# Kernel optimization log

Hardware: AMD Instinct MI355X
Metric: run time of the kernel (lower is better)

Reference implementation:

```python
import jax, jax.numpy as jnp
import numpy as np

N_NODES = 50000
N_EDGES = 800000
D_NODE = 128
D_EDGE = 128
D_OUT = 256
HID = 256


def setup_inputs() -> dict:
    key = jax.random.key(0)
    ks = jax.random.split(key, 10)
    s1 = 1.0 / np.sqrt(D_NODE + D_EDGE)
    s2 = 1.0 / np.sqrt(HID)
    s3 = 1.0 / np.sqrt(D_NODE + HID)
    return {
        "x": jax.random.normal(ks[0], (N_NODES, D_NODE), dtype=jnp.float32),
        "edge_index": jax.random.randint(ks[1], (2, N_EDGES), 0, N_NODES, dtype=jnp.int64),
        "edge_attr": jax.random.normal(ks[2], (N_EDGES, D_EDGE), dtype=jnp.float32),
        "u": jax.random.normal(ks[3], (1, 64), dtype=jnp.float32),
        "batch": jnp.zeros((N_NODES,), dtype=jnp.int64),
        "w1a": jax.random.normal(ks[4], (D_NODE + D_EDGE, HID), dtype=jnp.float32) * s1,
        "b1a": jnp.zeros((HID,), dtype=jnp.float32),
        "w1b": jax.random.normal(ks[5], (HID, HID), dtype=jnp.float32) * s2,
        "b1b": jnp.zeros((HID,), dtype=jnp.float32),
        "w2a": jax.random.normal(ks[6], (D_NODE + HID, HID), dtype=jnp.float32) * s3,
        "b2a": jnp.zeros((HID,), dtype=jnp.float32),
        "w2b": jax.random.normal(ks[7], (HID, D_OUT), dtype=jnp.float32) * s2,
        "b2b": jnp.zeros((D_OUT,), dtype=jnp.float32),
    }


def reference(x, edge_index, edge_attr, u, batch, w1a, b1a, w1b, b1b, w2a, b2a, w2b, b2b):
    row, col = edge_index[0], edge_index[1]
    # edge-wise MLP: [E, D_NODE + D_EDGE] -> 256 -> 256
    h = jnp.concatenate([x[row], edge_attr], axis=1)
    h = jax.nn.elu(h @ w1a + b1a) @ w1b + b1b  # [E, 256]
    # scatter_mean over destination nodes (dim_size = N)
    n = x.shape[0]
    sums = jax.ops.segment_sum(h, col, num_segments=n)  # [N, 256]
    cnt = jax.ops.segment_sum(jnp.ones((h.shape[0],), h.dtype), col, num_segments=n)
    mean = sums / jnp.maximum(cnt, 1.0)[:, None]
    # node-wise MLP: [N, D_NODE + 256] -> 256 -> D_OUT
    z = jnp.concatenate([x, mean], axis=1)
    return jax.nn.elu(z @ w2a + b2a) @ w2b + b2b
```

## Files before the change

kernel.cpp:

```cpp
#include <hip/hip_runtime.h>
#include <hip/hip_bf16.h>

#define N_NODES 50000
#define N_EDGES 800000

typedef short s16x8 __attribute__((ext_vector_type(8)));
typedef short s16x4 __attribute__((ext_vector_type(4)));
typedef float f32x4 __attribute__((ext_vector_type(4)));
typedef unsigned int u32x2 __attribute__((ext_vector_type(2)));

__device__ __forceinline__ unsigned short f2bf(float f) {
    union { float f; unsigned u; } v; v.f = f;
    unsigned r = v.u + 0x7fffu + ((v.u >> 16) & 1u);
    return (unsigned short)(r >> 16);
}

__device__ __forceinline__ unsigned cvt_pk_bf16(float a, float b) {
    unsigned r;
    asm("v_cvt_pk_bf16_f32 %0, %1, %2" : "=v"(r) : "v"(a), "v"(b));
    return r;
}

__device__ __forceinline__ s16x8 ld8(const unsigned short* p) {
    return *(const s16x8*)p;
}

__device__ __forceinline__ float elu(float h) {
    return h > 0.0f ? h : (__expf(h) - 1.0f);
}

__global__ void wconv_kernel(const float* __restrict__ src,
                             unsigned short* __restrict__ dst,
                             int K, int N) {
    int idx = blockIdx.x * 256 + threadIdx.x;
    if (idx >= K * N) return;
    int n = idx / K;
    int k = idx - n * K;
    dst[idx] = f2bf(src[k * N + n]);
}

__global__ void hist_kernel(const int* __restrict__ ei, int* __restrict__ hist) {
    int e = blockIdx.x * 256 + threadIdx.x;
    if (e < N_EDGES) atomicAdd(&hist[ei[N_EDGES + e]], 1);
}

__global__ void scan_kernel(const int* __restrict__ hist, int* __restrict__ cursor) {
    __shared__ int wsum[16];
    const int t = threadIdx.x;
    const int lane = t & 63, wv = t >> 6;
    const int CHUNK = 52;
    const int base = t * CHUNK;

    int s = 0;
    for (int i = 0; i < CHUNK; i += 4) {
        int idx = base + i;
        if (idx + 3 < N_NODES) {
            int4 v = *(const int4*)&hist[idx];
            s += v.x + v.y + v.z + v.w;
        } else {
#pragma unroll
            for (int j = 0; j < 4; j++)
                if (idx + j < N_NODES) s += hist[idx + j];
        }
    }
    int incl = s;
#pragma unroll
    for (int off = 1; off < 64; off <<= 1) {
        int o = __shfl_up(incl, off);
        if (lane >= off) incl += o;
    }
    if (lane == 63) wsum[wv] = incl;
    __syncthreads();
    if (t == 0) {
        int c = 0;
#pragma unroll
        for (int w = 0; w < 16; w++) { int v = wsum[w]; wsum[w] = c; c += v; }
    }
    __syncthreads();
    int excl = wsum[wv] + (incl - s);

    for (int i = 0; i < CHUNK; i += 4) {
        int idx = base + i;
        if (idx + 3 < N_NODES) {
            int4 v = *(const int4*)&hist[idx];
            int4 o;
            o.x = excl;
            o.y = o.x + v.x;
            o.z = o.y + v.y;
            o.w = o.z + v.z;
            *(int4*)&cursor[idx] = o;
            excl = o.w + v.w;
        } else {
#pragma unroll
            for (int j = 0; j < 4; j++)
                if (idx + j < N_NODES) { cursor[idx + j] = excl; excl += hist[idx + j]; }
        }
    }
}

__global__ void scatter_kernel(const int* __restrict__ ei, int* __restrict__ cursor,
                               int* __restrict__ sidx) {
    int e = blockIdx.x * 256 + threadIdx.x;
    if (e >= N_EDGES) return;
    int c = ei[N_EDGES + e];
    int p = atomicAdd(&cursor[c], 1);
    sidx[p] = e;
}

#define EP 264

__global__ __launch_bounds__(256, 4) void edge_kernel(
    const float* __restrict__ x, const int* __restrict__ ei,
    const float* __restrict__ ea, const int* __restrict__ sidx,
    const float* __restrict__ b1a,
    const unsigned short* __restrict__ w1aT,
    float* __restrict__ sums)
{
    __shared__ unsigned short lA[64 * EP];
    __shared__ int lrow[64];
    __shared__ int lidx[64];
    __shared__ int lsegcol[64];
    __shared__ unsigned char lsegid[64] __attribute__((aligned(4)));
    __shared__ int lnseg;
    const int t = threadIdx.x;
    const int e0 = blockIdx.x * 64;

    if (t < 64) {
        int idx = sidx[e0 + t];
        int r = ei[idx];
        int c = ei[N_EDGES + idx];
        lidx[t] = idx;
        lrow[t] = r;
        int cprev = __shfl_up(c, 1);
        int flag = (t == 0 || c != cprev) ? 1 : 0;
        unsigned long long m = __ballot(flag != 0);
        unsigned long long lm = (2ULL << t) - 1ULL;
        int sid = __popcll(m & lm) - 1;
        lsegid[t] = (unsigned char)sid;
        if (flag) lsegcol[sid] = c;
        if (t == 63) lnseg = __popcll(m);
    }
    __syncthreads();

    const f32x4* x4 = (const f32x4*)x;
    const f32x4* ea4 = (const f32x4*)ea;
#pragma unroll
    for (int i = 0; i < 8; i++) {
        int idx = i * 256 + t, r = idx >> 5, c4 = idx & 31;
        f32x4 v = x4[lrow[r] * 32 + c4];
        u32x2 b = { cvt_pk_bf16(v.x, v.y), cvt_pk_bf16(v.z, v.w) };
        *(u32x2*)&lA[r * EP + c4 * 4] = b;
    }
#pragma unroll
    for (int i = 0; i < 8; i++) {
        int idx = i * 256 + t, r = idx >> 5, c4 = idx & 31;
        f32x4 v = ea4[lidx[r] * 32 + c4];
        u32x2 b = { cvt_pk_bf16(v.x, v.y), cvt_pk_bf16(v.z, v.w) };
        *(u32x2*)&lA[r * EP + 128 + c4 * 4] = b;
    }
    __syncthreads();

    const int wv = t >> 6, lane = t & 63;
    const int quad = lane >> 4, l15 = lane & 15;

    f32x4 acc[4][4];
#pragma unroll
    for (int m = 0; m < 4; m++)
#pragma unroll
        for (int n = 0; n < 4; n++)
            acc[m][n] = (f32x4){0.f, 0.f, 0.f, 0.f};

    for (int kk = 0; kk < 8; kk++) {
        s16x8 a[4], b[4];
#pragma unroll
        for (int m = 0; m < 4; m++)
            a[m] = *(const s16x8*)&lA[(m * 16 + l15) * EP + kk * 32 + quad * 8];
#pragma unroll
        for (int n = 0; n < 4; n++)
            b[n] = ld8(&w1aT[(wv * 64 + n * 16 + l15) * 256 + kk * 32 + quad * 8]);
#pragma unroll
        for (int m = 0; m < 4; m++)
#pragma unroll
            for (int n = 0; n < 4; n++)
                acc[m][n] = __builtin_amdgcn_mfma_f32_16x16x32_bf16(a[m], b[n], acc[m][n], 0, 0, 0);
    }

#pragma unroll
    for (int n = 0; n < 4; n++) {
        float bias = b1a[wv * 64 + n * 16 + l15];
#pragma unroll
        for (int m = 0; m < 4; m++)
#pragma unroll
            for (int v = 0; v < 4; v++)
                acc[m][n][v] = elu(acc[m][n][v] + bias);
    }

    unsigned gm[4];
#pragma unroll
    for (int m = 0; m < 4; m++)
        gm[m] = *(const unsigned*)&lsegid[m * 16 + quad * 4];

    const int ns = lnseg;
    const int ocol = wv * 64 + quad * 16 + l15;
    for (int s = 0; s < ns; s++) {
        float p0 = 0.f, p1 = 0.f, p2 = 0.f, p3 = 0.f;
#pragma unroll
        for (int m = 0; m < 4; m++) {
#pragma unroll
            for (int v = 0; v < 4; v++) {
                if (((gm[m] >> (8 * v)) & 255u) == (unsigned)s) {
                    p0 += acc[m][0][v];
                    p1 += acc[m][1][v];
                    p2 += acc[m][2][v];
                    p3 += acc[m][3][v];
                }
            }
        }
        p0 += __shfl_xor(p0, 16); p0 += __shfl_xor(p0, 32);
        p1 += __shfl_xor(p1, 16); p1 += __shfl_xor(p1, 32);
        p2 += __shfl_xor(p2, 16); p2 += __shfl_xor(p2, 32);
        p3 += __shfl_xor(p3, 16); p3 += __shfl_xor(p3, 32);
        float val = (quad == 0) ? p0 : (quad == 1) ? p1 : ((quad == 2) ? p2 : p3);
        atomicAdd(&sums[lsegcol[s] * 256 + ocol], val);
    }
}

#define NP 392

__global__ __launch_bounds__(256, 3) void node_kernel(
    const float* __restrict__ x, const float* __restrict__ sums,
    const int* __restrict__ hist,
    const float* __restrict__ b1b, const float* __restrict__ b2a,
    const float* __restrict__ b2b,
    const unsigned short* __restrict__ w1bT, const unsigned short* __restrict__ w2aT,
    const unsigned short* __restrict__ w2bT,
    float* __restrict__ out)
{
    __shared__ unsigned short lZ[64 * NP];
    __shared__ float linv[64];
    __shared__ unsigned char lpos[64];
    const int t = threadIdx.x;
    const int n0 = blockIdx.x * 64;

    if (t < 64) {
        int c = 0;
        if (n0 + t < N_NODES) c = hist[n0 + t];
        lpos[t] = (c > 0);
        linv[t] = 1.0f / fmaxf((float)c, 1.0f);
    }
    __syncthreads();

#pragma unroll
    for (int i = 0; i < 8; i++) {
        int idx = i * 256 + t, r = idx >> 5, c4 = idx & 31;
        int node = n0 + r;
        f32x4 v = {0.f, 0.f, 0.f, 0.f};
        if (node < N_NODES) v = ((const f32x4*)x)[node * 32 + c4];
        u32x2 b = { cvt_pk_bf16(v.x, v.y), cvt_pk_bf16(v.z, v.w) };
        *(u32x2*)&lZ[r * NP + c4 * 4] = b;
    }
#pragma unroll
    for (int i = 0; i < 16; i++) {
        int idx = i * 256 + t, r = idx >> 6, c4 = idx & 63;
        int node = n0 + r;
        f32x4 v = {0.f, 0.f, 0.f, 0.f};
        if (node < N_NODES) v = ((const f32x4*)sums)[node * 64 + c4];
        float sc = linv[r];
        u32x2 b = { cvt_pk_bf16(v.x * sc, v.y * sc), cvt_pk_bf16(v.z * sc, v.w * sc) };
        *(u32x2*)&lZ[r * NP + 128 + c4 * 4] = b;
    }
    __syncthreads();

    const int wv = t >> 6, lane = t & 63;
    const int quad = lane >> 4, l15 = lane & 15;

    f32x4 acc[4][4];
#pragma unroll
    for (int m = 0; m < 4; m++)
#pragma unroll
        for (int n = 0; n < 4; n++)
            acc[m][n] = (f32x4){0.f, 0.f, 0.f, 0.f};

    for (int kk = 0; kk < 8; kk++) {
        s16x8 a[4], b[4];
#pragma unroll
        for (int m = 0; m < 4; m++)
            a[m] = *(const s16x8*)&lZ[(m * 16 + l15) * NP + 128 + kk * 32 + quad * 8];
#pragma unroll
        for (int n = 0; n < 4; n++)
            b[n] = ld8(&w1bT[(wv * 64 + n * 16 + l15) * 256 + kk * 32 + quad * 8]);
#pragma unroll
        for (int m = 0; m < 4; m++)
#pragma unroll
            for (int n = 0; n < 4; n++)
                acc[m][n] = __builtin_amdgcn_mfma_f32_16x16x32_bf16(a[m], b[n], acc[m][n], 0, 0, 0);
    }
    __syncthreads();

#pragma unroll
    for (int m = 0; m < 4; m++)
#pragma unroll
        for (int n = 0; n < 4; n++) {
            int col = wv * 64 + n * 16 + l15;
            float bias = b1b[col];
#pragma unroll
            for (int v = 0; v < 4; v++) {
                int row = m * 16 + quad * 4 + v;
                float h = acc[m][n][v] + (lpos[row] ? bias : 0.f);
                lZ[row * NP + 128 + col] = f2bf(h);
            }
            acc[m][n] = (f32x4){0.f, 0.f, 0.f, 0.f};
        }
    __syncthreads();

    for (int kk = 0; kk < 12; kk++) {
        s16x8 a[4], b[4];
#pragma unroll
        for (int m = 0; m < 4; m++)
            a[m] = *(const s16x8*)&lZ[(m * 16 + l15) * NP + kk * 32 + quad * 8];
#pragma unroll
        for (int n = 0; n < 4; n++)
            b[n] = ld8(&w2aT[(wv * 64 + n * 16 + l15) * 384 + kk * 32 + quad * 8]);
#pragma unroll
        for (int m = 0; m < 4; m++)
#pragma unroll
            for (int n = 0; n < 4; n++)
                acc[m][n] = __builtin_amdgcn_mfma_f32_16x16x32_bf16(a[m], b[n], acc[m][n], 0, 0, 0);
    }
    __syncthreads();

#pragma unroll
    for (int m = 0; m < 4; m++)
#pragma unroll
        for (int n = 0; n < 4; n++) {
            int col = wv * 64 + n * 16 + l15;
            float bias = b2a[col];
#pragma unroll
            for (int v = 0; v < 4; v++) {
                int row = m * 16 + quad * 4 + v;
                float h = elu(acc[m][n][v] + bias);
                lZ[row * NP + col] = f2bf(h);
            }
            acc[m][n] = (f32x4){0.f, 0.f, 0.f, 0.f};
        }
    __syncthreads();

    for (int kk = 0; kk < 8; kk++) {
        s16x8 a[4], b[4];
#pragma unroll
        for (int m = 0; m < 4; m++)
            a[m] = *(const s16x8*)&lZ[(m * 16 + l15) * NP + kk * 32 + quad * 8];
#pragma unroll
        for (int n = 0; n < 4; n++)
            b[n] = ld8(&w2bT[(wv * 64 + n * 16 + l15) * 256 + kk * 32 + quad * 8]);
#pragma unroll
        for (int m = 0; m < 4; m++)
#pragma unroll
            for (int n = 0; n < 4; n++)
                acc[m][n] = __builtin_amdgcn_mfma_f32_16x16x32_bf16(a[m], b[n], acc[m][n], 0, 0, 0);
    }

#pragma unroll
    for (int m = 0; m < 4; m++)
#pragma unroll
        for (int n = 0; n < 4; n++) {
            int col = wv * 64 + n * 16 + l15;
            float bias = b2b[col];
#pragma unroll
            for (int v = 0; v < 4; v++) {
                int row = m * 16 + quad * 4 + v;
                int node = n0 + row;
                if (node < N_NODES)
                    out[node * 256 + col] = acc[m][n][v] + bias;
            }
        }
}

#define WS_SUMS   0u
#define WS_HIST   51200000u
#define WS_ZERO_BYTES 51400000u
#define WS_CURSOR 51400000u
#define WS_SIDX   51600000u
#define WS_W1A    54800000u
#define WS_W1B    54931072u
#define WS_W2A    55062144u
#define WS_W2B    55258752u

extern "C" void kernel_launch(void* const* d_in, const int* in_sizes, int n_in,
                              void* d_out, int out_size, void* d_ws, size_t ws_size,
                              hipStream_t stream) {
    const float* x   = (const float*)d_in[0];
    const int*   ei  = (const int*)d_in[1];
    const float* ea  = (const float*)d_in[2];
    const float* w1a = (const float*)d_in[5];
    const float* b1a = (const float*)d_in[6];
    const float* w1b = (const float*)d_in[7];
    const float* b1b = (const float*)d_in[8];
    const float* w2a = (const float*)d_in[9];
    const float* b2a = (const float*)d_in[10];
    const float* w2b = (const float*)d_in[11];
    const float* b2b = (const float*)d_in[12];
    float* out = (float*)d_out;

    char* ws = (char*)d_ws;
    float* sums = (float*)(ws + WS_SUMS);
    int* hist   = (int*)(ws + WS_HIST);
    int* cursor = (int*)(ws + WS_CURSOR);
    int* sidx   = (int*)(ws + WS_SIDX);
    unsigned short* w1aT = (unsigned short*)(ws + WS_W1A);
    unsigned short* w1bT = (unsigned short*)(ws + WS_W1B);
    unsigned short* w2aT = (unsigned short*)(ws + WS_W2A);
    unsigned short* w2bT = (unsigned short*)(ws + WS_W2B);

    hipMemsetAsync(d_ws, 0, WS_ZERO_BYTES, stream);

    wconv_kernel<<<(256 * 256 + 255) / 256, 256, 0, stream>>>(w1a, w1aT, 256, 256);
    wconv_kernel<<<(256 * 256 + 255) / 256, 256, 0, stream>>>(w1b, w1bT, 256, 256);
    wconv_kernel<<<(384 * 256 + 255) / 256, 256, 0, stream>>>(w2a, w2aT, 384, 256);
    wconv_kernel<<<(256 * 256 + 255) / 256, 256, 0, stream>>>(w2b, w2bT, 256, 256);

    hist_kernel<<<(N_EDGES + 255) / 256, 256, 0, stream>>>(ei, hist);
    scan_kernel<<<1, 1024, 0, stream>>>(hist, cursor);
    scatter_kernel<<<(N_EDGES + 255) / 256, 256, 0, stream>>>(ei, cursor, sidx);

    edge_kernel<<<N_EDGES / 64, 256, 0, stream>>>(x, ei, ea, sidx, b1a, w1aT, sums);

    node_kernel<<<(N_NODES + 63) / 64, 256, 0, stream>>>(x, sums, hist, b1b, b2a, b2b,
                                                         w1bT, w2aT, w2bT, out);
}
```

Before: 976.7 us.

## Make edge kernel persistent with software-pipelined gather and double-buffered LDS

The edge kernel becomes persistent with 1024 blocks that loop over 64-edge tiles. The next tile's x/edge_attr gather is issued into registers during the current tile's epilogue, and index and segment metadata are prefetched two tiles ahead through a three-slot ring. The goal is to hide gather memory latency behind MFMA and atomic work instead of relying on many short-lived blocks. The cost is doubled LDS, larger register pressure from 16 f32x4 staging registers, and launch bounds lowered to 2 blocks per SIMD, which may cut occupancy.

```diff
diff --git a/kernel.cpp b/kernel.cpp
--- a/kernel.cpp
+++ b/kernel.cpp
@@ -3,6 +3,8 @@
 
 #define N_NODES 50000
 #define N_EDGES 800000
+#define NTILE   12500
+#define GRID_E  1024
 
 typedef short s16x8 __attribute__((ext_vector_type(8)));
 typedef short s16x4 __attribute__((ext_vector_type(4)));
@@ -109,119 +111,166 @@
 
 #define EP 264
 
-__global__ __launch_bounds__(256, 4) void edge_kernel(
+__global__ __launch_bounds__(256, 2) void edge_kernel(
     const float* __restrict__ x, const int* __restrict__ ei,
     const float* __restrict__ ea, const int* __restrict__ sidx,
     const float* __restrict__ b1a,
     const unsigned short* __restrict__ w1aT,
     float* __restrict__ sums)
 {
-    __shared__ unsigned short lA[64 * EP];
-    __shared__ int lrow[64];
-    __shared__ int lidx[64];
-    __shared__ int lsegcol[64];
-    __shared__ unsigned char lsegid[64] __attribute__((aligned(4)));
-    __shared__ int lnseg;
+    __shared__ unsigned short lA[2][64 * EP];
+    __shared__ int lrow[3][64];
+    __shared__ int lidx[3][64];
+    __shared__ int lsegcol[3][64];
+    __shared__ unsigned char lsegid[3][64] __attribute__((aligned(4)));
+    __shared__ int lnseg[3];
+
     const int t = threadIdx.x;
-    const int e0 = blockIdx.x * 64;
-
-    if (t < 64) {
-        int idx = sidx[e0 + t];
-        int r = ei[idx];
-        int c = ei[N_EDGES + idx];
-        lidx[t] = idx;
-        lrow[t] = r;
-        int cprev = __shfl_up(c, 1);
-        int flag = (t == 0 || c != cprev) ? 1 : 0;
-        unsigned long long m = __ballot(flag != 0);
-        unsigned long long lm = (2ULL << t) - 1ULL;
-        int sid = __popcll(m & lm) - 1;
-        lsegid[t] = (unsigned char)sid;
-        if (flag) lsegcol[sid] = c;
-        if (t == 63) lnseg = __popcll(m);
-    }
-    __syncthreads();
+    const int wv = t >> 6, lane = t & 63;
+    const int quad = lane >> 4, l15 = lane & 15;
+    const int b = blockIdx.x;
+    const int nj = (NTILE - b + GRID_E - 1) / GRID_E;
 
     const f32x4* x4 = (const f32x4*)x;
     const f32x4* ea4 = (const f32x4*)ea;
-#pragma unroll
-    for (int i = 0; i < 8; i++) {
-        int idx = i * 256 + t, r = idx >> 5, c4 = idx & 31;
-        f32x4 v = x4[lrow[r] * 32 + c4];
-        u32x2 b = { cvt_pk_bf16(v.x, v.y), cvt_pk_bf16(v.z, v.w) };
-        *(u32x2*)&lA[r * EP + c4 * 4] = b;
-    }
-#pragma unroll
-    for (int i = 0; i < 8; i++) {
-        int idx = i * 256 + t, r = idx >> 5, c4 = idx & 31;
-        f32x4 v = ea4[lidx[r] * 32 + c4];
-        u32x2 b = { cvt_pk_bf16(v.x, v.y), cvt_pk_bf16(v.z, v.w) };
-        *(u32x2*)&lA[r * EP + 128 + c4 * 4] = b;
-    }
-    __syncthreads();
-
-    const int wv = t >> 6, lane = t & 63;
-    const int quad = lane >> 4, l15 = lane & 15;
-
-    f32x4 acc[4][4];
-#pragma unroll
-    for (int m = 0; m < 4; m++)
-#pragma unroll
-        for (int n = 0; n < 4; n++)
-            acc[m][n] = (f32x4){0.f, 0.f, 0.f, 0.f};
-
-    for (int kk = 0; kk < 8; kk++) {
-        s16x8 a[4], b[4];
-#pragma unroll
-        for (int m = 0; m < 4; m++)
-            a[m] = *(const s16x8*)&lA[(m * 16 + l15) * EP + kk * 32 + quad * 8];
-#pragma unroll
-        for (int n = 0; n < 4; n++)
-            b[n] = ld8(&w1aT[(wv * 64 + n * 16 + l15) * 256 + kk * 32 + quad * 8]);
+
+    f32x4 xg[8], eg[8];
+
+    auto GATHER = [&](int sl) {
+#pragma unroll
+        for (int i = 0; i < 8; i++) {
+            int r = i * 8 + (t >> 5), c4 = t & 31;
+            xg[i] = x4[lrow[sl][r] * 32 + c4];
+            eg[i] = ea4[lidx[sl][r] * 32 + c4];
+        }
+    };
+    auto STORE = [&](int bf) {
+        unsigned short* dst = &lA[bf][0];
+#pragma unroll
+        for (int i = 0; i < 8; i++) {
+            int r = i * 8 + (t >> 5), c4 = t & 31;
+            *(u32x2*)&dst[r * EP + c4 * 4] =
+                (u32x2){ cvt_pk_bf16(xg[i].x, xg[i].y), cvt_pk_bf16(xg[i].z, xg[i].w) };
+            *(u32x2*)&dst[r * EP + 128 + c4 * 4] =
+                (u32x2){ cvt_pk_bf16(eg[i].x, eg[i].y), cvt_pk_bf16(eg[i].z, eg[i].w) };
+        }
+    };
+    auto COMMIT = [&](int sl, int id, int rw, int cl) {
+        int cprev = __shfl_up(cl, 1);
+        int flag = (lane == 0 || cl != cprev) ? 1 : 0;
+        unsigned long long m = __ballot(flag != 0);
+        unsigned long long lm = (2ULL << lane) - 1ULL;
+        int sid = __popcll(m & lm) - 1;
+        lidx[sl][lane] = id;
+        lrow[sl][lane] = rw;
+        lsegid[sl][lane] = (unsigned char)sid;
+        if (flag) lsegcol[sl][sid] = cl;
+        if (lane == 63) lnseg[sl] = __popcll(m);
+    };
+
+    int ridx = 0, rrow = 0, rcol = 0, sv = 0;
+    if (t < 64) {
+        int ia = sidx[(b             ) * 64 + lane];
+        int ib = sidx[(b +     GRID_E) * 64 + lane];
+        int ic = sidx[(b + 2 * GRID_E) * 64 + lane];
+        sv     = sidx[(b + 3 * GRID_E) * 64 + lane];
+        int ra = ei[ia], ca = ei[N_EDGES + ia];
+        int rb = ei[ib], cb = ei[N_EDGES + ib];
+        ridx = ic; rrow = ei[ic]; rcol = ei[N_EDGES + ic];
+        COMMIT(0, ia, ra, ca);
+        COMMIT(1, ib, rb, cb);
+    }
+    __syncthreads();
+    GATHER(0);
+    STORE(0);
+    __syncthreads();
+
+    float biasv[4];
+#pragma unroll
+    for (int n = 0; n < 4; n++) biasv[n] = b1a[wv * 64 + n * 16 + l15];
+
+    for (int j = 0; j < nj; j++) {
+        const int cs = j % 3, buf = j & 1;
+        const bool more = (j < nj - 1);
+
+        f32x4 acc[4][4];
 #pragma unroll
         for (int m = 0; m < 4; m++)
 #pragma unroll
             for (int n = 0; n < 4; n++)
-                acc[m][n] = __builtin_amdgcn_mfma_f32_16x16x32_bf16(a[m], b[n], acc[m][n], 0, 0, 0);
-    }
-
-#pragma unroll
-    for (int n = 0; n < 4; n++) {
-        float bias = b1a[wv * 64 + n * 16 + l15];
-#pragma unroll
-        for (int m = 0; m < 4; m++)
-#pragma unroll
-            for (int v = 0; v < 4; v++)
-                acc[m][n][v] = elu(acc[m][n][v] + bias);
-    }
-
-    unsigned gm[4];
-#pragma unroll
-    for (int m = 0; m < 4; m++)
-        gm[m] = *(const unsigned*)&lsegid[m * 16 + quad * 4];
-
-    const int ns = lnseg;
-    const int ocol = wv * 64 + quad * 16 + l15;
-    for (int s = 0; s < ns; s++) {
-        float p0 = 0.f, p1 = 0.f, p2 = 0.f, p3 = 0.f;
-#pragma unroll
-        for (int m = 0; m < 4; m++) {
-#pragma unroll
-            for (int v = 0; v < 4; v++) {
-                if (((gm[m] >> (8 * v)) & 255u) == (unsigned)s) {
-                    p0 += acc[m][0][v];
-                    p1 += acc[m][1][v];
-                    p2 += acc[m][2][v];
-                    p3 += acc[m][3][v];
+                acc[m][n] = (f32x4){0.f, 0.f, 0.f, 0.f};
+
+        const unsigned short* src = &lA[buf][0];
+        for (int kk = 0; kk < 8; kk++) {
+            s16x8 a[4], bw[4];
+#pragma unroll
+            for (int m = 0; m < 4; m++)
+                a[m] = *(const s16x8*)&src[(m * 16 + l15) * EP + kk * 32 + quad * 8];
+#pragma unroll
+            for (int n = 0; n < 4; n++)
+                bw[n] = ld8(&w1aT[(wv * 64 + n * 16 + l15) * 256 + kk * 32 + quad * 8]);
+#pragma unroll
+            for (int m = 0; m < 4; m++)
+#pragma unroll
+                for (int n = 0; n < 4; n++)
+                    acc[m][n] = __builtin_amdgcn_mfma_f32_16x16x32_bf16(a[m], bw[n], acc[m][n], 0, 0, 0);
+        }
+
+        if (more) GATHER((j + 1) % 3);
+
+        if (t < 64) {
+            int tl2 = b + (j + 2) * GRID_E;
+            if (tl2 < NTILE) {
+                COMMIT((j + 2) % 3, ridx, rrow, rcol);
+                if (tl2 + GRID_E < NTILE) {
+                    int id = sv;
+                    ridx = id; rrow = ei[id]; rcol = ei[N_EDGES + id];
+                    if (tl2 + 2 * GRID_E < NTILE)
+                        sv = sidx[(tl2 + 2 * GRID_E) * 64 + lane];
                 }
             }
         }
-        p0 += __shfl_xor(p0, 16); p0 += __shfl_xor(p0, 32);
-        p1 += __shfl_xor(p1, 16); p1 += __shfl_xor(p1, 32);
-        p2 += __shfl_xor(p2, 16); p2 += __shfl_xor(p2, 32);
-        p3 += __shfl_xor(p3, 16); p3 += __shfl_xor(p3, 32);
-        float val = (quad == 0) ? p0 : (quad == 1) ? p1 : ((quad == 2) ? p2 : p3);
-        atomicAdd(&sums[lsegcol[s] * 256 + ocol], val);
+
+#pragma unroll
+        for (int n = 0; n < 4; n++) {
+            float bias = biasv[n];
+#pragma unroll
+            for (int m = 0; m < 4; m++)
+#pragma unroll
+                for (int v = 0; v < 4; v++)
+                    acc[m][n][v] = elu(acc[m][n][v] + bias);
+        }
+
+        unsigned gm[4];
+#pragma unroll
+        for (int m = 0; m < 4; m++)
+            gm[m] = *(const unsigned*)&lsegid[cs][m * 16 + quad * 4];
+        const int ns = lnseg[cs];
+        const int ocol = wv * 64 + quad * 16 + l15;
+        for (int s = 0; s < ns; s++) {
+            float p0 = 0.f, p1 = 0.f, p2 = 0.f, p3 = 0.f;
+#pragma unroll
+            for (int m = 0; m < 4; m++) {
+#pragma unroll
+                for (int v = 0; v < 4; v++) {
+                    if (((gm[m] >> (8 * v)) & 255u) == (unsigned)s) {
+                        p0 += acc[m][0][v];
+                        p1 += acc[m][1][v];
+                        p2 += acc[m][2][v];
+                        p3 += acc[m][3][v];
+                    }
+                }
+            }
+            p0 += __shfl_xor(p0, 16); p0 += __shfl_xor(p0, 32);
+            p1 += __shfl_xor(p1, 16); p1 += __shfl_xor(p1, 32);
+            p2 += __shfl_xor(p2, 16); p2 += __shfl_xor(p2, 32);
+            p3 += __shfl_xor(p3, 16); p3 += __shfl_xor(p3, 32);
+            float val = (quad == 0) ? p0 : (quad == 1) ? p1 : ((quad == 2) ? p2 : p3);
+            atomicAdd(&sums[lsegcol[cs][s] * 256 + ocol], val);
+        }
+
+        if (more) STORE((j + 1) & 1);
+        __syncthreads();
     }
 }
 
@@ -423,7 +472,7 @@
     scan_kernel<<<1, 1024, 0, stream>>>(hist, cursor);
     scatter_kernel<<<(N_EDGES + 255) / 256, 256, 0, stream>>>(ei, cursor, sidx);
 
-    edge_kernel<<<N_EDGES / 64, 256, 0, stream>>>(x, ei, ea, sidx, b1a, w1aT, sums);
+    edge_kernel<<<GRID_E, 256, 0, stream>>>(x, ei, ea, sidx, b1a, w1aT, sums);
 
     node_kernel<<<(N_NODES + 63) / 64, 256, 0, stream>>>(x, sums, hist, b1b, b2a, b2b,
                                                          w1bT, w2aT, w2bT, out);
```

After: 1.266 ms. 1.3x slower.
